# Kernel tuning notes

Measured on AMD Instinct MI355X. Metric: run time of the kernel, lower is better.

Reference implementation:

```python
import jax, jax.numpy as jnp
import numpy as np

B, T, D = 16, 2048, 256
WINDOW = 128


def setup_inputs() -> dict:
    key = jax.random.key(0)
    ks = jax.random.split(key, 6)
    scale = 1.0 / np.sqrt(D)
    return {
        "x": jax.random.normal(ks[0], (B, T, D), dtype=jnp.float32),
        "Wq": jax.random.normal(ks[1], (D, D), dtype=jnp.float32) * scale,
        "Wk": jax.random.normal(ks[2], (D, D), dtype=jnp.float32) * scale,
        "Wv": jax.random.normal(ks[3], (D, D), dtype=jnp.float32) * scale,
        "Wo": jax.random.normal(ks[4], (D, D), dtype=jnp.float32) * scale,
        "w_bias": jax.random.normal(ks[5], (T, T), dtype=jnp.float32) * 0.1,
        "window": WINDOW,
    }


def reference(x, Wq, Wk, Wv, Wo, w_bias, window):
    # x: [B,T,D]; w_bias: [T,T] learned pairwise position bias.
    T_ = x.shape[1]
    q = jnp.einsum("btd,de->bte", x, Wq)
    k = jnp.einsum("btd,de->bte", x, Wk)
    v = jnp.einsum("btd,de->bte", x, Wv)

    # AFT-Local: bias is zeroed outside the local band |t - t'| < window,
    # but ALL positions still contribute (with bias 0) to the weighted sum.
    idx = jnp.arange(T_)
    band = jnp.abs(idx[:, None] - idx[None, :]) < window  # [T,T] bool
    w_local = jnp.where(band, w_bias, 0.0)

    # Stable exponentials: the num/den ratio is invariant to per-row shifts
    # of w and per-(b,d) shifts of k.
    w_stable = w_local - jnp.max(w_local, axis=1, keepdims=True)
    k_stable = k - jnp.max(k, axis=1, keepdims=True)
    expw = jnp.exp(w_stable)  # [T,T]
    expk = jnp.exp(k_stable)  # [B,T,D]

    num = jnp.einsum("ts,bsd->btd", expw, expk * v)
    den = jnp.einsum("ts,bsd->btd", expw, expk)
    y = jax.nn.sigmoid(q) * (num / den)
    return jnp.einsum("btd,de->bte", y, Wo)
```

## Files before the change

### kernel.cpp

```cpp
#include <hip/hip_runtime.h>
#include <math.h>

#define B_ 16
#define T_ 2048
#define D_ 256
#define W_ 128
#define M_ (B_*T_)

typedef __attribute__((ext_vector_type(8))) short bf16x8;
typedef __attribute__((ext_vector_type(4))) float f32x4;
typedef unsigned short u16;

static __device__ __forceinline__ u16 f32_bf16_rne(float f) {
    unsigned int u = __float_as_uint(f);
    u += 0x7FFF + ((u >> 16) & 1);
    return (u16)(u >> 16);
}
static __device__ __forceinline__ float bf16_f32(u16 h) {
    return __uint_as_float(((unsigned int)h) << 16);
}
static __device__ __forceinline__ void gload_lds16(const u16* g, u16* l) {
    __builtin_amdgcn_global_load_lds(
        (const __attribute__((address_space(1))) void*)g,
        (__attribute__((address_space(3))) void*)l, 16, 0, 0);
}

__global__ __launch_bounds__(256) void aft_split_wT(
    const float* __restrict__ Wq, const float* __restrict__ Wk,
    const float* __restrict__ Wv, const float* __restrict__ Wo,
    u16* __restrict__ Wth, u16* __restrict__ Wkl)
{
    __shared__ alignas(16) u16 Th[64][72];
    __shared__ alignas(16) u16 Tl[64][72];
    const float* Ws[4] = {Wq, Wk, Wv, Wo};
    const int mat = blockIdx.x;
    const float* W = Ws[mat];
    const int k0 = (blockIdx.y & 3) * 64;
    const int n0 = (blockIdx.y >> 2) * 64;
    const int tid = threadIdx.x;

    #pragma unroll
    for (int p = 0; p < 4; ++p) {
        const int k = p * 16 + (tid >> 4);
        const int n = (tid & 15) * 4;
        float4 v = *(const float4*)&W[(size_t)(k0 + k) * 256 + n0 + n];
        float vv[4] = {v.x, v.y, v.z, v.w};
        #pragma unroll
        for (int e = 0; e < 4; ++e) {
            u16 h = f32_bf16_rne(vv[e]);
            Th[n + e][k] = h;
            Tl[n + e][k] = f32_bf16_rne(vv[e] - bf16_f32(h));
        }
    }
    __syncthreads();

    const int n  = tid >> 2;
    const int kc = (tid & 3) * 16;
    size_t ob = ((size_t)mat * 256 + n0 + n) * 256 + k0 + kc;
    *(uint4*)&Wth[ob]     = *(const uint4*)&Th[n][kc];
    *(uint4*)&Wth[ob + 8] = *(const uint4*)&Th[n][kc + 8];
    if (mat == 1) {
        size_t ol = ((size_t)(n0 + n)) * 256 + k0 + kc;
        *(uint4*)&Wkl[ol]     = *(const uint4*)&Tl[n][kc];
        *(uint4*)&Wkl[ol + 8] = *(const uint4*)&Tl[n][kc + 8];
    }
}

__global__ void aft_ewb(const float* __restrict__ wb, u16* __restrict__ EWb)
{
    const int t = blockIdx.x;
    const int j = threadIdx.x;
    const int s = (t & ~63) - 128 + j;
    const int dlt = s - t;
    float v = 0.f;
    if (s >= 0 && s < T_ && dlt > -W_ && dlt < W_)
        v = expf(wb[(size_t)t * T_ + s]) - 1.0f;
    EWb[(size_t)t * 320 + j] = f32_bf16_rne(v);
}

__global__ __launch_bounds__(256) void aft_xsplit(
    const float* __restrict__ x, u16* __restrict__ xh, u16* __restrict__ xl)
{
    const size_t i0 = ((size_t)blockIdx.x * 256 + threadIdx.x) * 8;
    union { uint4 v; u16 h[8]; } H, L;
    #pragma unroll
    for (int c = 0; c < 2; ++c) {
        float4 v = *(const float4*)&x[i0 + c * 4];
        float vv[4] = {v.x, v.y, v.z, v.w};
        #pragma unroll
        for (int e = 0; e < 4; ++e) {
            u16 h = f32_bf16_rne(vv[e]);
            H.h[c * 4 + e] = h;
            L.h[c * 4 + e] = f32_bf16_rne(vv[e] - bf16_f32(h));
        }
    }
    *(uint4*)&xh[i0] = H.v;
    *(uint4*)&xl[i0] = L.v;
}

__global__ __launch_bounds__(256) void aft_qkv_mfma(
    const u16* __restrict__ xh, const u16* __restrict__ xl,
    const u16* __restrict__ Wth, const u16* __restrict__ Wkl,
    u16* __restrict__ ekT, u16* __restrict__ sigqT)
{
    __shared__ alignas(16) u16 sm[16384];
    u16* Ah = sm;
    u16* Al = sm + 4096;
    u16* Bs = sm + 8192;
    u16* Tr = sm;

    const int tid  = threadIdx.x;
    const int row0 = blockIdx.x * 128;
    const int col0 = blockIdx.y * 64;
    const int b    = row0 >> 11;
    const int t0g  = row0 & (T_ - 1);
    const int lane = tid & 63;
    const int wid  = tid >> 6;
    const int wm   = (wid & 1) * 64;
    const int wn   = (wid >> 1) * 32;
    const int qd   = lane >> 4;
    const int r    = lane & 15;

    f32x4 accq[4][2], acck[4][2], accv[4][2];
    #pragma unroll
    for (int i = 0; i < 4; ++i)
        #pragma unroll
        for (int j = 0; j < 2; ++j) {
            accq[i][j] = (f32x4){0.f, 0.f, 0.f, 0.f};
            acck[i][j] = accq[i][j];
            accv[i][j] = accq[i][j];
        }

    const int crow  = tid >> 2;
    const int ccol  = (tid & 3) * 8;
    const int wbase = wid * 512;

    const u16* Wsrc[4] = { Wth, Wth + 65536, Wkl, Wth + 2 * 65536 };

    for (int k0 = 0; k0 < D_; k0 += 32) {
        if (k0) __syncthreads();
        #pragma unroll
        for (int i = 0; i < 2; ++i) {
            size_t g = (size_t)(row0 + i * 64 + crow) * 256 + k0 + ccol;
            gload_lds16(&xh[g], &Ah[i * 2048 + wbase]);
            gload_lds16(&xl[g], &Al[i * 2048 + wbase]);
        }
        {
            size_t g = (size_t)(col0 + crow) * 256 + k0 + ccol;
            #pragma unroll
            for (int j = 0; j < 4; ++j)
                gload_lds16(&Wsrc[j][g], &Bs[j * 2048 + wbase]);
        }
        __syncthreads();

        bf16x8 ah[4], al[4];
        #pragma unroll
        for (int mf = 0; mf < 4; ++mf) {
            ah[mf] = *(const bf16x8*)&Ah[(wm + mf * 16 + r) * 32 + qd * 8];
            al[mf] = *(const bf16x8*)&Al[(wm + mf * 16 + r) * 32 + qd * 8];
        }
        #pragma unroll
        for (int nf = 0; nf < 2; ++nf) {
            int br = (wn + nf * 16 + r) * 32 + qd * 8;
            bf16x8 bq  = *(const bf16x8*)&Bs[br];
            bf16x8 bkh = *(const bf16x8*)&Bs[2048 + br];
            bf16x8 bkl = *(const bf16x8*)&Bs[4096 + br];
            bf16x8 bv  = *(const bf16x8*)&Bs[6144 + br];
            #pragma unroll
            for (int mf = 0; mf < 4; ++mf) {
                accq[mf][nf] = __builtin_amdgcn_mfma_f32_16x16x32_bf16(ah[mf], bq,  accq[mf][nf], 0, 0, 0);
                acck[mf][nf] = __builtin_amdgcn_mfma_f32_16x16x32_bf16(ah[mf], bkh, acck[mf][nf], 0, 0, 0);
                acck[mf][nf] = __builtin_amdgcn_mfma_f32_16x16x32_bf16(ah[mf], bkl, acck[mf][nf], 0, 0, 0);
                acck[mf][nf] = __builtin_amdgcn_mfma_f32_16x16x32_bf16(al[mf], bkh, acck[mf][nf], 0, 0, 0);
                accv[mf][nf] = __builtin_amdgcn_mfma_f32_16x16x32_bf16(ah[mf], bv,  accv[mf][nf], 0, 0, 0);
            }
        }
    }

    const int dl_r = tid >> 2;
    const int tseg = (tid & 3) * 32;
    #pragma unroll
    for (int round = 0; round < 3; ++round) {
        __syncthreads();
        #pragma unroll
        for (int mf = 0; mf < 4; ++mf) {
            #pragma unroll
            for (int nf = 0; nf < 2; ++nf) {
                ushort4 o;
                float vals[4];
                #pragma unroll
                for (int reg = 0; reg < 4; ++reg) {
                    if (round == 0)      vals[reg] = expf(acck[mf][nf][reg]);
                    else if (round == 1) vals[reg] = expf(acck[mf][nf][reg]) * accv[mf][nf][reg];
                    else                 vals[reg] = 1.f / (1.f + expf(-accq[mf][nf][reg]));
                }
                o.x = f32_bf16_rne(vals[0]); o.y = f32_bf16_rne(vals[1]);
                o.z = f32_bf16_rne(vals[2]); o.w = f32_bf16_rne(vals[3]);
                int dl = wn + nf * 16 + r;
                int tt = wm + mf * 16 + qd * 4;
                *(ushort4*)&Tr[dl * 136 + tt] = o;
            }
        }
        __syncthreads();
        u16* dst;
        if (round == 0)      dst = ekT   + ((size_t)(b * 512 + col0 + dl_r)) * 2048;
        else if (round == 1) dst = ekT   + ((size_t)(b * 512 + 256 + col0 + dl_r)) * 2048;
        else                 dst = sigqT + ((size_t)(b * 256 + col0 + dl_r)) * 2048;
        dst += t0g + tseg;
        const u16* srcp = &Tr[dl_r * 136 + tseg];
        #pragma unroll
        for (int i = 0; i < 4; ++i)
            *(uint4*)&dst[i * 8] = *(const uint4*)&srcp[i * 8];
    }
}

__global__ __launch_bounds__(256) void aft_sums(
    const u16* __restrict__ ekT, float* __restrict__ Sk, float* __restrict__ Sv)
{
    const int wid  = threadIdx.x >> 6;
    const int lane = threadIdx.x & 63;
    const int row  = blockIdx.x * 4 + wid;
    const int b = row >> 9, n = row & 511;
    const u16* p = ekT + (size_t)row * 2048 + lane * 32;
    float s = 0.f;
    #pragma unroll
    for (int c = 0; c < 4; ++c) {
        union { uint4 v; u16 h[8]; } u;
        u.v = *(const uint4*)&p[c * 8];
        #pragma unroll
        for (int i = 0; i < 8; ++i) s += bf16_f32(u.h[i]);
    }
    #pragma unroll
    for (int off = 32; off >= 1; off >>= 1) s += __shfl_down(s, off, 64);
    if (lane == 0) {
        if (n < 256) Sk[b * 256 + n] = s;
        else         Sv[b * 256 + n - 256] = s;
    }
}

__global__ __launch_bounds__(256) void aft_band_mfma(
    const u16* __restrict__ EWb, const u16* __restrict__ ekT,
    const u16* __restrict__ sigqT,
    const float* __restrict__ Sk, const float* __restrict__ Sv,
    u16* __restrict__ yTD)
{
    __shared__ alignas(16) u16 sm[12800];
    u16* Aw  = sm;
    u16* Bkv = sm + 2560;

    const int tid  = threadIdx.x;
    const int t0   = blockIdx.x * 64;
    const int b    = blockIdx.y >> 1;
    const int dh   = (blockIdx.y & 1) * 128;
    const int lane = tid & 63;
    const int wid  = tid >> 6;
    const int wn   = wid * 32;
    const int qd   = lane >> 4;
    const int r    = lane & 15;

    f32x4 accn[4][2], accd[4][2];
    #pragma unroll
    for (int i = 0; i < 4; ++i)
        #pragma unroll
        for (int j = 0; j < 2; ++j) {
            accn[i][j] = (f32x4){0.f, 0.f, 0.f, 0.f};
            accd[i][j] = (f32x4){0.f, 0.f, 0.f, 0.f};
        }

    const int atl = tid >> 2;
    const int ak8 = (tid & 3) * 8;

    for (int c = 0; c < 10; ++c) {
        const int sc = t0 - 128 + c * 32;
        if (sc < 0 || sc >= T_) continue;
        __syncthreads();
        *(uint4*)&Aw[atl * 40 + ak8] =
            *(const uint4*)&EWb[(size_t)(t0 + atl) * 320 + c * 32 + ak8];
        #pragma unroll
        for (int rr = 0; rr < 4; ++rr) {
            int nl = rr * 64 + atl;
            int n  = (nl < 128) ? (dh + nl) : (256 + dh + nl - 128);
            *(uint4*)&Bkv[nl * 40 + ak8] =
                *(const uint4*)&ekT[((size_t)(b * 512) + n) * 2048 + sc + ak8];
        }
        __syncthreads();

        bf16x8 af[4];
        #pragma unroll
        for (int mf = 0; mf < 4; ++mf)
            af[mf] = *(const bf16x8*)&Aw[(mf * 16 + r) * 40 + qd * 8];
        #pragma unroll
        for (int nf = 0; nf < 2; ++nf) {
            bf16x8 be = *(const bf16x8*)&Bkv[(wn + nf * 16 + r) * 40 + qd * 8];
            bf16x8 bv = *(const bf16x8*)&Bkv[(128 + wn + nf * 16 + r) * 40 + qd * 8];
            #pragma unroll
            for (int mf = 0; mf < 4; ++mf) {
                accd[mf][nf] = __builtin_amdgcn_mfma_f32_16x16x32_bf16(af[mf], be, accd[mf][nf], 0, 0, 0);
                accn[mf][nf] = __builtin_amdgcn_mfma_f32_16x16x32_bf16(af[mf], bv, accn[mf][nf], 0, 0, 0);
            }
        }
    }

    __syncthreads();
    u16* Ly = sm;
    #pragma unroll
    for (int nf = 0; nf < 2; ++nf) {
        const int dl = wn + nf * 16 + r;
        const int d  = dh + dl;
        const float skq = Sk[(b << 8) + d];
        const float svq = Sv[(b << 8) + d];
        #pragma unroll
        for (int mf = 0; mf < 4; ++mf) {
            const int tt = t0 + mf * 16 + qd * 4;
            size_t off = ((size_t)(b << 8) + d) * 2048 + tt;
            ushort4 sg = *(const ushort4*)&sigqT[off];
            float s4[4] = {bf16_f32(sg.x), bf16_f32(sg.y), bf16_f32(sg.z), bf16_f32(sg.w)};
            #pragma unroll
            for (int reg = 0; reg < 4; ++reg) {
                float y = s4[reg] * (svq + accn[mf][nf][reg]) / (skq + accd[mf][nf][reg]);
                Ly[(mf * 16 + qd * 4 + reg) * 136 + dl] = f32_bf16_rne(y);
            }
        }
    }
    __syncthreads();
    {
        const int tl  = tid >> 2;
        const int ds4 = (tid & 3) * 32;
        u16* dst = yTD + ((size_t)b * 2048 + t0 + tl) * 256 + dh + ds4;
        #pragma unroll
        for (int i = 0; i < 4; ++i)
            *(uint4*)&dst[i * 8] = *(const uint4*)&Ly[tl * 136 + ds4 + i * 8];
    }
}

__global__ __launch_bounds__(256) void aft_out_mfma(
    const u16* __restrict__ yTD, const u16* __restrict__ Woth,
    float* __restrict__ out)
{
    __shared__ alignas(16) u16 sm[7680];
    u16* As = sm;
    u16* Bh = sm + 2560;

    const int tid  = threadIdx.x;
    const int row0 = blockIdx.x * 64;
    const int col0 = blockIdx.y * 128;
    const int lane = tid & 63;
    const int wid  = tid >> 6;
    const int wn   = wid * 32;
    const int qd   = lane >> 4;
    const int r    = lane & 15;

    f32x4 acc[4][2];
    #pragma unroll
    for (int i = 0; i < 4; ++i)
        #pragma unroll
        for (int j = 0; j < 2; ++j)
            acc[i][j] = (f32x4){0.f, 0.f, 0.f, 0.f};

    const int arow = tid >> 2;
    const int aseg = (tid & 3) * 8;
    const int brw  = tid >> 1;
    const int bsg  = (tid & 1) * 16;

    for (int k0 = 0; k0 < D_; k0 += 32) {
        {
            uint4 v = *(const uint4*)&yTD[(size_t)(row0 + arow) * 256 + k0 + aseg];
            *(uint4*)&As[arow * 40 + aseg] = v;
        }
        {
            size_t g = (size_t)(col0 + brw) * 256 + k0 + bsg;
            uint4 v0 = *(const uint4*)&Woth[g];
            uint4 v1 = *(const uint4*)&Woth[g + 8];
            *(uint4*)&Bh[brw * 40 + bsg]     = v0;
            *(uint4*)&Bh[brw * 40 + bsg + 8] = v1;
        }
        __syncthreads();

        bf16x8 af[4];
        #pragma unroll
        for (int mf = 0; mf < 4; ++mf)
            af[mf] = *(const bf16x8*)&As[(mf * 16 + r) * 40 + qd * 8];
        #pragma unroll
        for (int nf = 0; nf < 2; ++nf) {
            bf16x8 bh = *(const bf16x8*)&Bh[(wn + nf * 16 + r) * 40 + qd * 8];
            #pragma unroll
            for (int mf = 0; mf < 4; ++mf)
                acc[mf][nf] = __builtin_amdgcn_mfma_f32_16x16x32_bf16(af[mf], bh, acc[mf][nf], 0, 0, 0);
        }
        __syncthreads();
    }

    #pragma unroll
    for (int mf = 0; mf < 4; ++mf)
        #pragma unroll
        for (int nf = 0; nf < 2; ++nf)
            #pragma unroll
            for (int reg = 0; reg < 4; ++reg) {
                int mrow = row0 + mf * 16 + qd * 4 + reg;
                int ncol = col0 + wn + nf * 16 + r;
                out[(size_t)mrow * D_ + ncol] = acc[mf][nf][reg];
            }
}

extern "C" void kernel_launch(void* const* d_in, const int* in_sizes, int n_in,
                              void* d_out, int out_size, void* d_ws, size_t ws_size,
                              hipStream_t stream)
{
    const float* x  = (const float*)d_in[0];
    const float* Wq = (const float*)d_in[1];
    const float* Wk = (const float*)d_in[2];
    const float* Wv = (const float*)d_in[3];
    const float* Wo = (const float*)d_in[4];
    const float* wb = (const float*)d_in[5];

    u16* Wth   = (u16*)d_ws;
    u16* Wkl   = Wth + 262144;
    u16* EWb   = Wkl + 65536;
    u16* ekT   = EWb + 655360;
    u16* sigqT = ekT + 16777216;
    u16* yTD   = sigqT + 8388608;
    float* Sk  = (float*)(yTD + 8388608);
    float* Sv  = Sk + 4096;
    u16* xl    = (u16*)(Sv + 4096);
    u16* xh    = yTD;

    aft_split_wT<<<dim3(4, 16), 256, 0, stream>>>(Wq, Wk, Wv, Wo, Wth, Wkl);
    aft_ewb<<<dim3(T_), 320, 0, stream>>>(wb, EWb);
    aft_xsplit<<<dim3(M_ * D_ / (256 * 8)), 256, 0, stream>>>(x, xh, xl);
    aft_qkv_mfma<<<dim3(M_ / 128, 4), 256, 0, stream>>>(xh, xl, Wth, Wkl, ekT, sigqT);
    aft_sums<<<dim3(8192 / 4), 256, 0, stream>>>(ekT, Sk, Sv);
    aft_band_mfma<<<dim3(T_ / 64, B_ * 2), 256, 0, stream>>>(EWb, ekT, sigqT, Sk, Sv, yTD);
    aft_out_mfma<<<dim3(M_ / 64, 2), 256, 0, stream>>>(yTD, Wth + 3 * 65536, (float*)d_out);
}
```

Baseline: 210.1 us.

## Fuse x bf16 hi/lo split into QKV GEMM with larger swizzled tiles

Removes the separate kernel that split x into bf16 high and low halves. The QKV GEMM now loads fp32 x itself, converts it to hi/lo bf16 in registers and writes it into LDS, which avoids a round trip of the split activations through global memory. The GEMM block grows to 512 threads covering a 128x128 tile, so x is re-read by only two column blocks instead of four. An XOR swizzle is added to the LDS layout to reduce bank conflicts. The trade-offs are more LDS per block, conversion work inside the GEMM's load phase, and direct fp32 loads replacing the async global-to-LDS loads for the A operand.

```diff
diff --git a/kernel.cpp b/kernel.cpp
--- a/kernel.cpp
+++ b/kernel.cpp
@@ -78,32 +78,12 @@
     EWb[(size_t)t * 320 + j] = f32_bf16_rne(v);
 }
 
-__global__ __launch_bounds__(256) void aft_xsplit(
-    const float* __restrict__ x, u16* __restrict__ xh, u16* __restrict__ xl)
-{
-    const size_t i0 = ((size_t)blockIdx.x * 256 + threadIdx.x) * 8;
-    union { uint4 v; u16 h[8]; } H, L;
-    #pragma unroll
-    for (int c = 0; c < 2; ++c) {
-        float4 v = *(const float4*)&x[i0 + c * 4];
-        float vv[4] = {v.x, v.y, v.z, v.w};
-        #pragma unroll
-        for (int e = 0; e < 4; ++e) {
-            u16 h = f32_bf16_rne(vv[e]);
-            H.h[c * 4 + e] = h;
-            L.h[c * 4 + e] = f32_bf16_rne(vv[e] - bf16_f32(h));
-        }
-    }
-    *(uint4*)&xh[i0] = H.v;
-    *(uint4*)&xl[i0] = L.v;
-}
-
-__global__ __launch_bounds__(256) void aft_qkv_mfma(
-    const u16* __restrict__ xh, const u16* __restrict__ xl,
+__global__ __launch_bounds__(512, 4) void aft_qkv_mfma(
+    const float* __restrict__ x,
     const u16* __restrict__ Wth, const u16* __restrict__ Wkl,
     u16* __restrict__ ekT, u16* __restrict__ sigqT)
 {
-    __shared__ alignas(16) u16 sm[16384];
+    __shared__ alignas(16) u16 sm[34816];
     u16* Ah = sm;
     u16* Al = sm + 4096;
     u16* Bs = sm + 8192;
@@ -111,63 +91,76 @@
 
     const int tid  = threadIdx.x;
     const int row0 = blockIdx.x * 128;
-    const int col0 = blockIdx.y * 64;
+    const int col0 = blockIdx.y * 128;
     const int b    = row0 >> 11;
     const int t0g  = row0 & (T_ - 1);
     const int lane = tid & 63;
     const int wid  = tid >> 6;
-    const int wm   = (wid & 1) * 64;
-    const int wn   = (wid >> 1) * 32;
+    const int wm   = (wid & 3) * 32;
+    const int wn   = (wid >> 2) * 64;
     const int qd   = lane >> 4;
     const int r    = lane & 15;
 
-    f32x4 accq[4][2], acck[4][2], accv[4][2];
-    #pragma unroll
-    for (int i = 0; i < 4; ++i)
-        #pragma unroll
-        for (int j = 0; j < 2; ++j) {
+    f32x4 accq[2][4], acck[2][4], accv[2][4];
+    #pragma unroll
+    for (int i = 0; i < 2; ++i)
+        #pragma unroll
+        for (int j = 0; j < 4; ++j) {
             accq[i][j] = (f32x4){0.f, 0.f, 0.f, 0.f};
             acck[i][j] = accq[i][j];
             accv[i][j] = accq[i][j];
         }
 
     const int crow  = tid >> 2;
-    const int ccol  = (tid & 3) * 8;
+    const int cswz  = (crow >> 1) & 3;
+    const int gchk  = tid & 3;
+    const int ccols = (gchk ^ cswz) * 8;
+    const int aslot = crow * 32 + (gchk ^ cswz) * 8;
     const int wbase = wid * 512;
-
-    const u16* Wsrc[4] = { Wth, Wth + 65536, Wkl, Wth + 2 * 65536 };
+    const int sq8   = (qd ^ ((r >> 1) & 3)) * 8;
 
     for (int k0 = 0; k0 < D_; k0 += 32) {
         if (k0) __syncthreads();
-        #pragma unroll
-        for (int i = 0; i < 2; ++i) {
-            size_t g = (size_t)(row0 + i * 64 + crow) * 256 + k0 + ccol;
-            gload_lds16(&xh[g], &Ah[i * 2048 + wbase]);
-            gload_lds16(&xl[g], &Al[i * 2048 + wbase]);
-        }
         {
-            size_t g = (size_t)(col0 + crow) * 256 + k0 + ccol;
-            #pragma unroll
-            for (int j = 0; j < 4; ++j)
-                gload_lds16(&Wsrc[j][g], &Bs[j * 2048 + wbase]);
-        }
-        __syncthreads();
-
-        bf16x8 ah[4], al[4];
-        #pragma unroll
-        for (int mf = 0; mf < 4; ++mf) {
-            ah[mf] = *(const bf16x8*)&Ah[(wm + mf * 16 + r) * 32 + qd * 8];
-            al[mf] = *(const bf16x8*)&Al[(wm + mf * 16 + r) * 32 + qd * 8];
-        }
-        #pragma unroll
-        for (int nf = 0; nf < 2; ++nf) {
-            int br = (wn + nf * 16 + r) * 32 + qd * 8;
+            size_t gb = (size_t)(col0 + crow) * 256 + k0 + ccols;
+            gload_lds16(&Wth[gb],          &Bs[0 * 4096 + wbase]);
+            gload_lds16(&Wth[65536 + gb],  &Bs[1 * 4096 + wbase]);
+            gload_lds16(&Wkl[gb],          &Bs[2 * 4096 + wbase]);
+            gload_lds16(&Wth[131072 + gb], &Bs[3 * 4096 + wbase]);
+        }
+        {
+            size_t ga = (size_t)(row0 + crow) * 256 + k0 + gchk * 8;
+            float4 v0 = *(const float4*)&x[ga];
+            float4 v1 = *(const float4*)&x[ga + 4];
+            float vv[8] = {v0.x, v0.y, v0.z, v0.w, v1.x, v1.y, v1.z, v1.w};
+            union { uint4 q; u16 h[8]; } H, L;
+            #pragma unroll
+            for (int e = 0; e < 8; ++e) {
+                u16 h = f32_bf16_rne(vv[e]);
+                H.h[e] = h;
+                L.h[e] = f32_bf16_rne(vv[e] - bf16_f32(h));
+            }
+            *(uint4*)&Ah[aslot] = H.q;
+            *(uint4*)&Al[aslot] = L.q;
+        }
+        __syncthreads();
+
+        bf16x8 ah[2], al[2];
+        #pragma unroll
+        for (int mf = 0; mf < 2; ++mf) {
+            int ar = (wm + mf * 16 + r) * 32 + sq8;
+            ah[mf] = *(const bf16x8*)&Ah[ar];
+            al[mf] = *(const bf16x8*)&Al[ar];
+        }
+        #pragma unroll
+        for (int nf = 0; nf < 4; ++nf) {
+            int br = (wn + nf * 16 + r) * 32 + sq8;
             bf16x8 bq  = *(const bf16x8*)&Bs[br];
-            bf16x8 bkh = *(const bf16x8*)&Bs[2048 + br];
-            bf16x8 bkl = *(const bf16x8*)&Bs[4096 + br];
-            bf16x8 bv  = *(const bf16x8*)&Bs[6144 + br];
-            #pragma unroll
-            for (int mf = 0; mf < 4; ++mf) {
+            bf16x8 bkh = *(const bf16x8*)&Bs[4096 + br];
+            bf16x8 bkl = *(const bf16x8*)&Bs[8192 + br];
+            bf16x8 bv  = *(const bf16x8*)&Bs[12288 + br];
+            #pragma unroll
+            for (int mf = 0; mf < 2; ++mf) {
                 accq[mf][nf] = __builtin_amdgcn_mfma_f32_16x16x32_bf16(ah[mf], bq,  accq[mf][nf], 0, 0, 0);
                 acck[mf][nf] = __builtin_amdgcn_mfma_f32_16x16x32_bf16(ah[mf], bkh, acck[mf][nf], 0, 0, 0);
                 acck[mf][nf] = __builtin_amdgcn_mfma_f32_16x16x32_bf16(ah[mf], bkl, acck[mf][nf], 0, 0, 0);
@@ -183,9 +176,9 @@
     for (int round = 0; round < 3; ++round) {
         __syncthreads();
         #pragma unroll
-        for (int mf = 0; mf < 4; ++mf) {
-            #pragma unroll
-            for (int nf = 0; nf < 2; ++nf) {
+        for (int mf = 0; mf < 2; ++mf) {
+            #pragma unroll
+            for (int nf = 0; nf < 4; ++nf) {
                 ushort4 o;
                 float vals[4];
                 #pragma unroll
@@ -421,13 +414,10 @@
     u16* yTD   = sigqT + 8388608;
     float* Sk  = (float*)(yTD + 8388608);
     float* Sv  = Sk + 4096;
-    u16* xl    = (u16*)(Sv + 4096);
-    u16* xh    = yTD;
 
     aft_split_wT<<<dim3(4, 16), 256, 0, stream>>>(Wq, Wk, Wv, Wo, Wth, Wkl);
     aft_ewb<<<dim3(T_), 320, 0, stream>>>(wb, EWb);
-    aft_xsplit<<<dim3(M_ * D_ / (256 * 8)), 256, 0, stream>>>(x, xh, xl);
-    aft_qkv_mfma<<<dim3(M_ / 128, 4), 256, 0, stream>>>(xh, xl, Wth, Wkl, ekT, sigqT);
+    aft_qkv_mfma<<<dim3(M_ / 128, 2), 512, 0, stream>>>(x, Wth, Wkl, ekT, sigqT);
     aft_sums<<<dim3(8192 / 4), 256, 0, stream>>>(ekT, Sk, Sv);
     aft_band_mfma<<<dim3(T_ / 64, B_ * 2), 256, 0, stream>>>(EWb, ekT, sigqT, Sk, Sv, yTD);
     aft_out_mfma<<<dim3(M_ / 64, 2), 256, 0, stream>>>(yTD, Wth + 3 * 65536, (float*)d_out);
```

Result: slower. 229.4 us (+9.2%).
